# Kernel tuning notes

Hardware: AMD Instinct MI355X
Metric: run time of the kernel (lower is better)

Reference implementation:

```python
import jax, jax.numpy as jnp
from jax import lax
import numpy as np

V, D, H, CO = 50000, 300, 512, 100
B, S, W = 64, 32, 128


def setup_inputs() -> dict:
    key = jax.random.key(0)
    ks = jax.random.split(key, 24)
    sc = 0.1  # mimic uniform(-0.1, 0.1)-style small init; keeps tanh unsaturated
    inp = {
        "paragraphs": jax.random.randint(ks[0], (B, S, W), 0, V, dtype=jnp.int64),
        "embed_table": jax.random.normal(ks[1], (V, D), jnp.float32),
        "conv_w3": jax.random.normal(ks[2], (CO, 1, 3, D), jnp.float32) * 0.05,
        "conv_b3": jax.random.normal(ks[3], (CO,), jnp.float32) * sc,
        "conv_w4": jax.random.normal(ks[4], (CO, 1, 4, D), jnp.float32) * 0.05,
        "conv_b4": jax.random.normal(ks[5], (CO,), jnp.float32) * sc,
        "conv_w5": jax.random.normal(ks[6], (CO, 1, 5, D), jnp.float32) * 0.05,
        "conv_b5": jax.random.normal(ks[7], (CO,), jnp.float32) * sc,
        "proj_w": jax.random.normal(ks[8], (300, 300), jnp.float32) * sc,
        "proj_b": jax.random.normal(ks[9], (300,), jnp.float32) * sc,
        "init_w": jax.random.normal(ks[10], (H, 300), jnp.float32) * sc,
        "init_b": jax.random.normal(ks[11], (H,), jnp.float32) * sc,
        "w_ih_f": jax.random.normal(ks[12], (H, 300), jnp.float32) * sc,
        "w_hh_f": jax.random.normal(ks[13], (H, H), jnp.float32) * sc,
        "b_ih_f": jax.random.normal(ks[14], (H,), jnp.float32) * sc,
        "b_hh_f": jax.random.normal(ks[15], (H,), jnp.float32) * sc,
        "w_ih_b": jax.random.normal(ks[16], (H, 300), jnp.float32) * sc,
        "w_hh_b": jax.random.normal(ks[17], (H, H), jnp.float32) * sc,
        "b_ih_b": jax.random.normal(ks[18], (H,), jnp.float32) * sc,
        "b_hh_b": jax.random.normal(ks[19], (H,), jnp.float32) * sc,
        "cls_w": jax.random.normal(ks[20], (5, 2 * H), jnp.float32) * sc,
        "cls_b": jax.random.normal(ks[21], (5,), jnp.float32) * sc,
    }
    return inp


def _cnn_text(tok, embed_table, conv_params):
    # tok: (N, W) int ids -> (N, 3*CO) sentence features (dropout = eval identity)
    emb = embed_table[tok]              # (N, W, D)
    x = emb[:, None, :, :]              # (N, 1, W, D)
    feats = []
    for w, b in conv_params:
        y = lax.conv_general_dilated(
            x, w, window_strides=(1, 1), padding="VALID",
            dimension_numbers=("NCHW", "OIHW", "NCHW"))  # (N, CO, W-K+1, 1)
        y = jax.nn.relu(y[..., 0] + b[None, :, None])       # (N, CO, W-K+1)
        feats.append(jnp.max(y, axis=2))                    # (N, CO) max-pool over time
    return jnp.concatenate(feats, axis=1)                    # (N, 3*CO)


def reference(paragraphs, embed_table, conv_w3, conv_b3, conv_w4, conv_b4,
              conv_w5, conv_b5, proj_w, proj_b, init_w, init_b,
              w_ih_f, w_hh_f, b_ih_f, b_hh_f, w_ih_b, w_hh_b, b_ih_b, b_hh_b,
              cls_w, cls_b):
    b_, s_, w_ = paragraphs.shape
    tok = paragraphs.reshape(b_ * s_, w_)
    conv_params = [(conv_w3, conv_b3), (conv_w4, conv_b4), (conv_w5, conv_b5)]
    sent = _cnn_text(tok, embed_table, conv_params).reshape(b_, s_, 3 * CO)

    # init_rnn: same init hidden for both directions
    h0 = sent[:, 0, :] @ init_w.T + init_b  # (B, H)

    def step(carry, x_t):
        hf, hb = carry
        xi = x_t @ proj_w.T + proj_b  # (B, 300)
        hf_n = jnp.tanh(xi @ w_ih_f.T + b_ih_f + hf @ w_hh_f.T + b_hh_f)
        hb_n = jnp.tanh(xi @ w_ih_b.T + b_ih_b + hb @ w_hh_b.T + b_hh_b)
        pred = jnp.concatenate([hf_n, hb_n], axis=1) @ cls_w.T + cls_b  # (B, 5)
        return (hf_n, hb_n), pred

    _, preds = lax.scan(step, (h0, h0), jnp.swapaxes(sent, 0, 1))  # (S, B, 5)
    return jnp.swapaxes(preds, 0, 1)  # (B, S, 5)
```

## Files before the change

kernel.cpp:

```cpp
#include <hip/hip_runtime.h>


#define LDSK     304
#define LDSROWB  608
#define LDSBYTES 80256

typedef __bf16   bf16x8 __attribute__((ext_vector_type(8)));
typedef float    f32x16 __attribute__((ext_vector_type(16)));
typedef _Float16 h2v    __attribute__((ext_vector_type(2)));

#define MFMA32(a, b, c) __builtin_amdgcn_mfma_f32_32x32x16_bf16((a), (b), (c), 0, 0, 0)

__global__ void prep_emb(const float* __restrict__ e, __bf16* __restrict__ eh) {
  long i = ((long)blockIdx.x * 256 + threadIdx.x) * 8;
  if (i >= 15000000L) return;
  float4 a = *(const float4*)(e + i);
  float4 b = *(const float4*)(e + i + 4);
  union { __bf16 h[8]; uint4 u; } pk;
  pk.h[0] = (__bf16)a.x; pk.h[1] = (__bf16)a.y; pk.h[2] = (__bf16)a.z; pk.h[3] = (__bf16)a.w;
  pk.h[4] = (__bf16)b.x; pk.h[5] = (__bf16)b.y; pk.h[6] = (__bf16)b.z; pk.h[7] = (__bf16)b.w;
  *(uint4*)(eh + i) = pk.u;
}

__global__ void prep_convw(const float* __restrict__ w3, const float* __restrict__ w4,
                           const float* __restrict__ w5, __bf16* __restrict__ Aw32) {
  int idx = blockIdx.x * 256 + threadIdx.x;
  if (idx >= 48 * 19 * 64 * 8) return;
  int i    = idx & 7;
  int lane = (idx >> 3) & 63;
  int rem  = idx >> 9;
  int ks   = rem % 19, g = rem / 19;
  int kc, cg, j; const float* w;
  if (g < 12)      { kc = 3; cg = g / 3;        j = g % 3;        w = w3; }
  else if (g < 28) { kc = 4; cg = (g - 12) / 4; j = (g - 12) % 4; w = w4; }
  else             { kc = 5; cg = (g - 28) / 5; j = (g - 28) % 5; w = w5; }
  int ch = cg * 32 + (lane & 31);
  int k  = ks * 16 + (lane >> 5) * 8 + i;
  float v = 0.f;
  if (ch < 100 && k < 300) v = w[(ch * kc + j) * 300 + k];
  Aw32[idx] = (__bf16)v;
}

__device__ __forceinline__ unsigned int packf16(float a, float b) {
  h2v h; h[0] = (_Float16)a; h[1] = (_Float16)b;
  return __builtin_bit_cast(unsigned int, h);
}
__global__ void prep_whh(const float* __restrict__ whf, const float* __restrict__ whb,
                         uint4* __restrict__ Wq) {
  int idx = blockIdx.x * 256 + threadIdx.x;
  if (idx >= 2 * 128 * 256) return;
  int dir = idx >> 15;
  int rem = idx & 32767;
  int kq = rem >> 8, tid = rem & 255;
  const float* W = dir ? whb : whf;
  const float* r0 = W + (size_t)tid * 512 + 4 * kq;
  const float* r1 = W + (size_t)(tid + 256) * 512 + 4 * kq;
  uint4 o;
  o.x = packf16(r0[0], r0[1]);
  o.y = packf16(r1[0], r1[1]);
  o.z = packf16(r0[2], r0[3]);
  o.w = packf16(r1[2], r1[3]);
  Wq[idx] = o;
}

__device__ __forceinline__ void conv_chunk32(const char* ldsc, const __bf16* __restrict__ Aw32,
                                             int GB, int kc, int cg0,
                                             const float* __restrict__ bias,
                                             int colbase, int pmax,
                                             float* __restrict__ srow, int lane) {
  const int m32 = lane & 31, hi = lane >> 5;
  f32x16 acc[2][4];
#pragma unroll
  for (int i = 0; i < 2; ++i)
#pragma unroll
    for (int n = 0; n < 4; ++n)
#pragma unroll
      for (int e = 0; e < 16; ++e) acc[i][n][e] = 0.f;

  for (int j = 0; j < kc; ++j) {
    const int row0 = m32 + j;
    const int mask = (row0 & 7) << 4;
    const int rowbyte = row0 * LDSROWB + hi * 16;
    const __bf16* a0 = Aw32 + (size_t)(GB + cg0 * kc + j) * (19 * 512) + lane * 8;
    const __bf16* a1 = Aw32 + (size_t)(GB + (cg0 + 1) * kc + j) * (19 * 512) + lane * 8;
#pragma unroll 2
    for (int ks = 0; ks < 19; ++ks) {
      bf16x8 bf[4];
#pragma unroll
      for (int nt = 0; nt < 4; ++nt) {
        int addr = rowbyte + nt * (32 * LDSROWB) + ks * 32;
        bf[nt] = *(const bf16x8*)(ldsc + (addr ^ mask));
      }
      bf16x8 af0 = *(const bf16x8*)(a0 + ks * 512);
      bf16x8 af1 = *(const bf16x8*)(a1 + ks * 512);
#pragma unroll
      for (int nt = 0; nt < 4; ++nt)
        acc[0][nt] = MFMA32(af0, bf[nt], acc[0][nt]);
#pragma unroll
      for (int nt = 0; nt < 4; ++nt)
        acc[1][nt] = MFMA32(af1, bf[nt], acc[1][nt]);
    }
  }
#pragma unroll
  for (int i = 0; i < 2; ++i) {
    float m[16];
#pragma unroll
    for (int r = 0; r < 16; ++r) m[r] = -3.0e38f;
#pragma unroll
    for (int nt = 0; nt < 4; ++nt) {
      int p = nt * 32 + m32;
      bool valid = (p <= pmax);
#pragma unroll
      for (int r = 0; r < 16; ++r)
        m[r] = fmaxf(m[r], valid ? acc[i][nt][r] : -3.0e38f);
    }
#pragma unroll
    for (int r = 0; r < 16; ++r) {
#pragma unroll
      for (int d = 1; d < 32; d <<= 1) m[r] = fmaxf(m[r], __shfl_xor(m[r], d, 64));
    }
    if (m32 == 0) {
#pragma unroll
      for (int r = 0; r < 16; ++r) {
        int ch = (cg0 + i) * 32 + (r & 3) + 8 * (r >> 2) + 4 * hi;
        if (ch < 100) srow[colbase + ch] = fmaxf(m[r] + bias[ch], 0.f);
      }
    }
  }
}

__global__ void __launch_bounds__(256, 2)
conv_kernel(const int* __restrict__ tok, const __bf16* __restrict__ embh,
            const __bf16* __restrict__ Aw32,
            const float* __restrict__ b3, const float* __restrict__ b4, const float* __restrict__ b5,
            float* __restrict__ sent) {
  extern __shared__ __bf16 lds[];
  char* ldsc = (char*)lds;
  const int sid = blockIdx.x, tid = threadIdx.x;
  const int* t0 = tok + sid * 128;
  const char* eb = (const char*)embh;
  for (int i = tid; i < 4 * 76; i += 256) {
    int r = 128 + i / 76, q = i - (i / 76) * 76;
    *(uint2*)(ldsc + ((r * LDSROWB + q * 8) ^ ((r & 7) << 4))) = (uint2){0u, 0u};
  }
  if (tid < 128) {
    *(uint2*)(ldsc + ((tid * LDSROWB + 600) ^ ((tid & 7) << 4))) = (uint2){0u, 0u};
  }
  for (int i = tid; i < 128 * 75; i += 256) {
    int r = i / 75, q = i - r * 75;
    long tk = (long)t0[r];
    uint2 v = *(const uint2*)(eb + tk * 600L + q * 8);
    *(uint2*)(ldsc + ((r * LDSROWB + q * 8) ^ ((r & 7) << 4))) = v;
  }
  __syncthreads();
  const int wave = tid >> 6, lane = tid & 63;
  float* srow = sent + (size_t)sid * 304;
  switch (wave) {
    case 0:
      conv_chunk32(ldsc, Aw32, 28, 5, 0, b5, 200, 123, srow, lane);
      break;
    case 1:
      conv_chunk32(ldsc, Aw32, 28, 5, 2, b5, 200, 123, srow, lane);
      break;
    case 2:
      conv_chunk32(ldsc, Aw32, 12, 4, 0, b4, 100, 124, srow, lane);
      conv_chunk32(ldsc, Aw32,  0, 3, 0, b3,   0, 125, srow, lane);
      break;
    default:
      conv_chunk32(ldsc, Aw32, 12, 4, 2, b4, 100, 124, srow, lane);
      conv_chunk32(ldsc, Aw32,  0, 3, 2, b3,   0, 125, srow, lane);
      break;
  }
}

__global__ void xigh0_kernel(const float* __restrict__ sent,
                             const float* __restrict__ pw, const float* __restrict__ pb,
                             const float* __restrict__ wf, const float* __restrict__ wb,
                             const float* __restrict__ bif, const float* __restrict__ bhf,
                             const float* __restrict__ bib, const float* __restrict__ bhb,
                             const float* __restrict__ iw, const float* __restrict__ ib,
                             float* __restrict__ G, float* __restrict__ h0) {
  __shared__ float s[8][300];
  __shared__ float xi[8][304];
  const int tid = threadIdx.x;
  if (blockIdx.x < 256) {
    const int rb = blockIdx.x * 8;
    for (int i = tid; i < 8 * 300; i += 256) {
      int r = i / 300, c = i - r * 300;
      s[r][c] = sent[(size_t)(rb + r) * 304 + c];
    }
    __syncthreads();
    for (int o = tid; o < 300; o += 256) {
      const float* w = pw + o * 300;
      float bvv = pb[o];
      float a[8];
#pragma unroll
      for (int r = 0; r < 8; ++r) a[r] = bvv;
      for (int k = 0; k < 300; k += 4) {
        float4 wv = *(const float4*)(w + k);
#pragma unroll
        for (int r = 0; r < 8; ++r)
          a[r] += wv.x * s[r][k] + wv.y * s[r][k + 1] + wv.z * s[r][k + 2] + wv.w * s[r][k + 3];
      }
#pragma unroll
      for (int r = 0; r < 8; ++r) xi[r][o] = a[r];
    }
    __syncthreads();
    for (int o = tid; o < 1024; o += 256) {
      int dir = o >> 9, oo = o & 511;
      const float* w = (dir ? wb : wf) + oo * 300;
      float bvv = dir ? (bib[oo] + bhb[oo]) : (bif[oo] + bhf[oo]);
      float a[8];
#pragma unroll
      for (int r = 0; r < 8; ++r) a[r] = bvv;
      for (int k = 0; k < 300; k += 4) {
        float4 wv = *(const float4*)(w + k);
#pragma unroll
        for (int r = 0; r < 8; ++r)
          a[r] += wv.x * xi[r][k] + wv.y * xi[r][k + 1] + wv.z * xi[r][k + 2] + wv.w * xi[r][k + 3];
      }
#pragma unroll
      for (int r = 0; r < 8; ++r) G[(rb + r) * 1024 + o] = a[r];
    }
  } else {
    const int bb = (blockIdx.x - 256) * 8;
    for (int i = tid; i < 8 * 300; i += 256) {
      int r = i / 300, c = i - r * 300;
      s[r][c] = sent[(size_t)((bb + r) * 32) * 304 + c];
    }
    __syncthreads();
    for (int o = tid; o < 512; o += 256) {
      const float* w = iw + o * 300;
      float bvv = ib[o];
      float a[8];
#pragma unroll
      for (int r = 0; r < 8; ++r) a[r] = bvv;
      for (int k = 0; k < 300; k += 4) {
        float4 wv = *(const float4*)(w + k);
#pragma unroll
        for (int r = 0; r < 8; ++r)
          a[r] += wv.x * s[r][k] + wv.y * s[r][k + 1] + wv.z * s[r][k + 2] + wv.w * s[r][k + 3];
      }
#pragma unroll
      for (int r = 0; r < 8; ++r) h0[(bb + r) * 512 + o] = a[r];
    }
  }
}

#if __has_builtin(__builtin_amdgcn_fdot2)
#define FDOT2(a, b, c) __builtin_amdgcn_fdot2((a), (b), (c), false)
#else
static __device__ __forceinline__ float FDOT2(h2v a, h2v b, float c) {
  return c + (float)a[0] * (float)b[0] + (float)a[1] * (float)b[1];
}
#endif
__device__ __forceinline__ h2v as_h2(unsigned int u) { return __builtin_bit_cast(h2v, u); }

__global__ void __launch_bounds__(512)
rnn_kernel(const uint4* __restrict__ Wq, const float* __restrict__ G,
           const float* __restrict__ h0, float* __restrict__ H) {
  const int blk = blockIdx.x, tid = threadIdx.x;
  const int dir = blk >> 6, b = blk & 63;
  const int o = tid & 255, kh = tid >> 8;
  __shared__ float hs[512];
  __shared__ uint2 h2p[128];
  __shared__ float part[2][512];
  if (tid < 512) { hs[tid] = h0[b * 512 + tid]; }
  __syncthreads();
  const uint4* W = Wq + (size_t)dir * (128 * 256);
  for (int t = 0; t < 32; ++t) {
    if (tid < 256) ((unsigned int*)h2p)[tid] = packf16(hs[2 * tid], hs[2 * tid + 1]);
    __syncthreads();
    float a0 = 0.f, a1 = 0.f, c0 = 0.f, c1 = 0.f;
    const int kbase = kh * 64;
#pragma unroll 4
    for (int kk = 0; kk < 64; kk += 2) {
      int k0 = kbase + kk, k1 = k0 + 1;
      uint4 w0 = W[k0 * 256 + o]; uint2 p0 = h2p[k0];
      uint4 w1 = W[k1 * 256 + o]; uint2 p1 = h2p[k1];
      a0 = FDOT2(as_h2(w0.x), as_h2(p0.x), a0); a0 = FDOT2(as_h2(w0.z), as_h2(p0.y), a0);
      a1 = FDOT2(as_h2(w0.y), as_h2(p0.x), a1); a1 = FDOT2(as_h2(w0.w), as_h2(p0.y), a1);
      c0 = FDOT2(as_h2(w1.x), as_h2(p1.x), c0); c0 = FDOT2(as_h2(w1.z), as_h2(p1.y), c0);
      c1 = FDOT2(as_h2(w1.y), as_h2(p1.x), c1); c1 = FDOT2(as_h2(w1.w), as_h2(p1.y), c1);
    }
    part[kh][o] = a0 + c0;
    part[kh][o + 256] = a1 + c1;
    __syncthreads();
    if (kh == 0) {
      const float* g = G + (size_t)(b * 32 + t) * 1024 + dir * 512;
      float n0 = tanhf(g[o]       + part[0][o]       + part[1][o]);
      float n1 = tanhf(g[o + 256] + part[0][o + 256] + part[1][o + 256]);
      hs[o] = n0; hs[o + 256] = n1;
      float* Ht = H + (size_t)((dir * 64 + b) * 32 + t) * 512;
      Ht[o] = n0; Ht[o + 256] = n1;
    }
    __syncthreads();
  }
}

__global__ void pred_kernel(const float* __restrict__ H, const float* __restrict__ cw,
                            const float* __restrict__ cb, float* __restrict__ out) {
  const int bt = blockIdx.x;
  const int lane = threadIdx.x;
  const int b = bt >> 5, t = bt & 31;
  const float* hf = H + ((size_t)(b * 32 + t)) * 512;
  const float* hb = H + ((size_t)((64 + b) * 32 + t)) * 512;
  for (int c = 0; c < 5; ++c) {
    const float* w = cw + c * 1024;
    float a = 0.f;
    for (int o = lane; o < 512; o += 64) a += w[o] * hf[o] + w[512 + o] * hb[o];
#pragma unroll
    for (int d = 32; d; d >>= 1) a += __shfl_down(a, d, 64);
    if (lane == 0) out[bt * 5 + c] = a + cb[c];
  }
}

extern "C" void kernel_launch(void* const* d_in, const int* in_sizes, int n_in,
                              void* d_out, int out_size, void* d_ws, size_t ws_size,
                              hipStream_t stream) {
  const int*   tok  = (const int*)d_in[0];
  const float* emb  = (const float*)d_in[1];
  const float* w3   = (const float*)d_in[2];
  const float* b3   = (const float*)d_in[3];
  const float* w4   = (const float*)d_in[4];
  const float* b4   = (const float*)d_in[5];
  const float* w5   = (const float*)d_in[6];
  const float* b5   = (const float*)d_in[7];
  const float* pw   = (const float*)d_in[8];
  const float* pb   = (const float*)d_in[9];
  const float* iw   = (const float*)d_in[10];
  const float* ib   = (const float*)d_in[11];
  const float* wihf = (const float*)d_in[12];
  const float* whhf = (const float*)d_in[13];
  const float* bihf = (const float*)d_in[14];
  const float* bhhf = (const float*)d_in[15];
  const float* wihb = (const float*)d_in[16];
  const float* whhb = (const float*)d_in[17];
  const float* bihb = (const float*)d_in[18];
  const float* bhhb = (const float*)d_in[19];
  const float* cw   = (const float*)d_in[20];
  const float* cb   = (const float*)d_in[21];
  float* out = (float*)d_out;

  char* ws = (char*)d_ws;
  __bf16* Aw32  = (__bf16*)(ws);
  uint4* Wq     = (uint4*)(ws +  1u * 1024 * 1024);
  float* sent   = (float*)(ws +  2u * 1024 * 1024);
  __bf16* embh  = (__bf16*)(ws + 8u * 1024 * 1024);
  float* G      = (float*)(ws +  8u * 1024 * 1024);
  float* h0     = (float*)(ws + 16u * 1024 * 1024);
  float* H      = (float*)(ws + 17u * 1024 * 1024);

  prep_emb<<<7325, 256, 0, stream>>>(emb, embh);
  prep_convw<<<1824, 256, 0, stream>>>(w3, w4, w5, Aw32);
  prep_whh<<<256, 256, 0, stream>>>(whhf, whhb, Wq);

  hipFuncSetAttribute(reinterpret_cast<const void*>(conv_kernel),
                      hipFuncAttributeMaxDynamicSharedMemorySize, LDSBYTES);
  conv_kernel<<<2048, 256, LDSBYTES, stream>>>(tok, embh, Aw32, b3, b4, b5, sent);

  xigh0_kernel<<<264, 256, 0, stream>>>(sent, pw, pb, wihf, wihb, bihf, bhhf, bihb, bhhb,
                                        iw, ib, G, h0);
  rnn_kernel<<<128, 512, 0, stream>>>(Wq, G, h0, H);
  pred_kernel<<<2048, 64, 0, stream>>>(H, cw, cb, out);
}
```

Measured before the change: 602.9 us.

## Process two batch rows per RNN block to reuse recurrent weights; batch pred blocks

The recurrent kernel now handles two batch elements per 1024-thread block. Each W_hh load is shared across both hidden states, and the K dimension is split four ways instead of two, halving the weight traffic per output. It launches 64 blocks instead of 128, which lowers parallelism across CUs for the latency-bound sequential loop. The prediction kernel also packs four (b,t) rows per 256-thread block to cut the number of tiny blocks.

Measured after the change: 609.8 us. Within noise of the previous version (+1.2%).

```diff
diff --git a/kernel.cpp b/kernel.cpp
--- a/kernel.cpp
+++ b/kernel.cpp
@@ -256,43 +256,50 @@
 #endif
 __device__ __forceinline__ h2v as_h2(unsigned int u) { return __builtin_bit_cast(h2v, u); }
 
-__global__ void __launch_bounds__(512)
+__global__ void __launch_bounds__(1024)
 rnn_kernel(const uint4* __restrict__ Wq, const float* __restrict__ G,
            const float* __restrict__ h0, float* __restrict__ H) {
   const int blk = blockIdx.x, tid = threadIdx.x;
-  const int dir = blk >> 6, b = blk & 63;
-  const int o = tid & 255, kh = tid >> 8;
-  __shared__ float hs[512];
-  __shared__ uint2 h2p[128];
-  __shared__ float part[2][512];
-  if (tid < 512) { hs[tid] = h0[b * 512 + tid]; }
+  const int dir = blk >> 5, b0 = (blk & 31) * 2;
+  const int o = tid & 255, kh = (tid >> 8) & 3;
+  __shared__ float hs[2][512];
+  __shared__ uint2 h2p[2][128];
+  __shared__ float part[4][2][512];
+  {
+    int c = tid >> 9, oo = tid & 511;
+    hs[c][oo] = h0[(b0 + c) * 512 + oo];
+  }
   __syncthreads();
   const uint4* W = Wq + (size_t)dir * (128 * 256);
   for (int t = 0; t < 32; ++t) {
-    if (tid < 256) ((unsigned int*)h2p)[tid] = packf16(hs[2 * tid], hs[2 * tid + 1]);
-    __syncthreads();
-    float a0 = 0.f, a1 = 0.f, c0 = 0.f, c1 = 0.f;
-    const int kbase = kh * 64;
+    if (tid < 256) {
+      int c = tid >> 7, kq = tid & 127;
+      h2p[c][kq] = (uint2){packf16(hs[c][4 * kq], hs[c][4 * kq + 1]),
+                           packf16(hs[c][4 * kq + 2], hs[c][4 * kq + 3])};
+    }
+    __syncthreads();
+    float a00 = 0.f, a01 = 0.f, a10 = 0.f, a11 = 0.f;
+    const int kb = kh * 32;
 #pragma unroll 4
-    for (int kk = 0; kk < 64; kk += 2) {
-      int k0 = kbase + kk, k1 = k0 + 1;
-      uint4 w0 = W[k0 * 256 + o]; uint2 p0 = h2p[k0];
-      uint4 w1 = W[k1 * 256 + o]; uint2 p1 = h2p[k1];
-      a0 = FDOT2(as_h2(w0.x), as_h2(p0.x), a0); a0 = FDOT2(as_h2(w0.z), as_h2(p0.y), a0);
-      a1 = FDOT2(as_h2(w0.y), as_h2(p0.x), a1); a1 = FDOT2(as_h2(w0.w), as_h2(p0.y), a1);
-      c0 = FDOT2(as_h2(w1.x), as_h2(p1.x), c0); c0 = FDOT2(as_h2(w1.z), as_h2(p1.y), c0);
-      c1 = FDOT2(as_h2(w1.y), as_h2(p1.x), c1); c1 = FDOT2(as_h2(w1.w), as_h2(p1.y), c1);
-    }
-    part[kh][o] = a0 + c0;
-    part[kh][o + 256] = a1 + c1;
-    __syncthreads();
-    if (kh == 0) {
-      const float* g = G + (size_t)(b * 32 + t) * 1024 + dir * 512;
-      float n0 = tanhf(g[o]       + part[0][o]       + part[1][o]);
-      float n1 = tanhf(g[o + 256] + part[0][o + 256] + part[1][o + 256]);
-      hs[o] = n0; hs[o + 256] = n1;
-      float* Ht = H + (size_t)((dir * 64 + b) * 32 + t) * 512;
-      Ht[o] = n0; Ht[o + 256] = n1;
+    for (int kk = 0; kk < 32; ++kk) {
+      int kq = kb + kk;
+      uint4 w = W[kq * 256 + o];
+      uint2 p0 = h2p[0][kq], p1 = h2p[1][kq];
+      a00 = FDOT2(as_h2(w.x), as_h2(p0.x), a00); a00 = FDOT2(as_h2(w.z), as_h2(p0.y), a00);
+      a01 = FDOT2(as_h2(w.y), as_h2(p0.x), a01); a01 = FDOT2(as_h2(w.w), as_h2(p0.y), a01);
+      a10 = FDOT2(as_h2(w.x), as_h2(p1.x), a10); a10 = FDOT2(as_h2(w.z), as_h2(p1.y), a10);
+      a11 = FDOT2(as_h2(w.y), as_h2(p1.x), a11); a11 = FDOT2(as_h2(w.w), as_h2(p1.y), a11);
+    }
+    part[kh][0][o] = a00; part[kh][0][o + 256] = a01;
+    part[kh][1][o] = a10; part[kh][1][o + 256] = a11;
+    __syncthreads();
+    {
+      int c = tid >> 9, oo = tid & 511;
+      const float* g = G + (size_t)((b0 + c) * 32 + t) * 1024 + dir * 512;
+      float s = g[oo] + ((part[0][c][oo] + part[1][c][oo]) + (part[2][c][oo] + part[3][c][oo]));
+      float n = tanhf(s);
+      hs[c][oo] = n;
+      H[(size_t)((dir * 64 + b0 + c) * 32 + t) * 512 + oo] = n;
     }
     __syncthreads();
   }
@@ -300,8 +307,8 @@
 
 __global__ void pred_kernel(const float* __restrict__ H, const float* __restrict__ cw,
                             const float* __restrict__ cb, float* __restrict__ out) {
-  const int bt = blockIdx.x;
-  const int lane = threadIdx.x;
+  const int bt = blockIdx.x * 4 + (threadIdx.x >> 6);
+  const int lane = threadIdx.x & 63;
   const int b = bt >> 5, t = bt & 31;
   const float* hf = H + ((size_t)(b * 32 + t)) * 512;
   const float* hb = H + ((size_t)((64 + b) * 32 + t)) * 512;
@@ -361,6 +368,6 @@
 
   xigh0_kernel<<<264, 256, 0, stream>>>(sent, pw, pb, wihf, wihb, bihf, bhhf, bihb, bhhb,
                                         iw, ib, G, h0);
-  rnn_kernel<<<128, 512, 0, stream>>>(Wq, G, h0, H);
-  pred_kernel<<<2048, 64, 0, stream>>>(H, cw, cb, out);
-}
+  rnn_kernel<<<64, 1024, 0, stream>>>(Wq, G, h0, H);
+  pred_kernel<<<512, 256, 0, stream>>>(H, cw, cb, out);
+}
```
